# Kernel tuning notes

Measured on AMD Instinct MI355X. Metric: run time of the kernel, lower is better.

The kernel has to match this reference:

```python
import jax, jax.numpy as jnp
import numpy as np


def setup_inputs() -> dict:
    key = jax.random.key(0)
    k0, k1 = jax.random.split(key)
    B, C, H, W = 8, 16, 512, 512
    im0 = jax.random.normal(k0, (B, C, H, W), dtype=jnp.float32)
    flow = jax.random.normal(k1, (B, H, W, 2), dtype=jnp.float32)
    im1 = jnp.zeros((B, C, H, W), dtype=jnp.float32)
    return {"im0": im0, "flow": flow, "im1": im1}


def _forward_warp_bilinear(im0, flow, im1):
    # im0: [B,C,H,W], flow: [B,H,W,2] (flow[...,0]=dx, flow[...,1]=dy), im1: [B,C,H,W]
    B, C, H, W = im0.shape
    gx = jnp.arange(W, dtype=flow.dtype)[None, None, :]   # [1,1,W]
    gy = jnp.arange(H, dtype=flow.dtype)[None, :, None]   # [1,H,1]
    x = gx + flow[..., 0]                                 # [B,H,W] dest x
    y = gy + flow[..., 1]                                 # [B,H,W] dest y

    x0f = jnp.floor(x)
    y0f = jnp.floor(y)
    x0 = x0f.astype(jnp.int32)
    y0 = y0f.astype(jnp.int32)
    x1 = x0 + 1
    y1 = y0 + 1

    # Original Python/CUDA kernel scatters only if ALL four corners are in-bounds.
    valid = (x0 >= 0) & (x1 <= W - 1) & (y0 >= 0) & (y1 <= H - 1)  # [B,H,W]

    fx = x - x0f   # in [0,1)
    fy = y - y0f
    w_nw = (1.0 - fx) * (1.0 - fy)
    w_ne = fx * (1.0 - fy)
    w_sw = (1.0 - fx) * fy
    w_se = fx * fy

    # channel-last flat layout for efficient scatter: [B, H*W, C]
    src = jnp.transpose(im0, (0, 2, 3, 1)).reshape(B, H * W, C)
    out = jnp.transpose(im1, (0, 2, 3, 1)).reshape(B, H * W, C)
    bb = jnp.arange(B)[:, None]                            # [B,1] broadcasts over H*W

    for yi, xi, wgt in ((y0, x0, w_nw), (y0, x1, w_ne),
                        (y1, x0, w_sw), (y1, x1, w_se)):
        t = jnp.where(valid, yi * W + xi, 0).reshape(B, H * W)          # safe indices
        wv = jnp.where(valid, wgt, 0.0).reshape(B, H * W)               # zeroed weights
        out = out.at[bb, t].add(wv[..., None] * src)
    return jnp.transpose(out.reshape(B, H, W, C), (0, 3, 1, 2))


def reference(im0, flow, im1):
    return _forward_warp_bilinear(im0, flow, im1)
```

## Files before the change

### kernel.cpp

```cpp
#include <hip/hip_runtime.h>


#define BB 8
#define CC 16
#define HH 512
#define WW 512
#define TIL 32
#define RAD 4
#define REG (TIL + 2*RAD)
#define NSRC (REG*REG)
#define NTHR 512
#define NREC ((NSRC + NTHR - 1) / NTHR)
#define NENT (NSRC * 4)
#define CB 2
#define NGRP (CC / CB)

__global__ __launch_bounds__(NTHR, 6) void fwarp_tile(
    const float* __restrict__ im0,
    const float* __restrict__ flow,
    float* __restrict__ out)
{
    __shared__ unsigned s_ent[NENT];
    __shared__ unsigned s_cur[TIL * TIL];
    __shared__ float2   s_img[NSRC];
    __shared__ unsigned s_wtot[8];

    const int tid = threadIdx.x;
    const int bid  = blockIdx.x;
    const int tile = ((bid & 7) << 8) | (bid >> 3);
    const int tcx = tile & 15;
    const int tcy = (tile >> 4) & 15;
    const int b   = tile >> 8;
    const int w0  = tcx * TIL;
    const int h0  = tcy * TIL;

    const float2* flow2 = (const float2*)flow + ((size_t)b << 18);

    float4 rw[NREC];
    int    rp0[NREC];
    int    rk[NREC];
    int    rgi[NREC];

    for (int j = tid; j < TIL * TIL; j += NTHR) s_cur[j] = 0u;

#pragma unroll
    for (int r = 0; r < NREC; ++r) {
        rk[r] = 0; rp0[r] = 0; rgi[r] = 0;
        rw[r] = make_float4(0.f, 0.f, 0.f, 0.f);
        const int i = tid + r * NTHR;
        if (i < NSRC) {
            const int ry = i / REG;
            const int rx = i - ry * REG;
            const int sy = h0 - RAD + ry;
            const int sx = w0 - RAD + rx;
            const bool inimg = (sx >= 0) & (sx < WW) & (sy >= 0) & (sy < HH);
            rgi[r] = inimg ? ((sy << 9) + sx) : 0;

            float fxv = 0.0f, fyv = 0.0f;
            if (inimg) {
                const float2 f = flow2[(sy << 9) + sx];
                fxv = f.x; fyv = f.y;
            }
            const float x = (float)sx + fxv;
            const float y = (float)sy + fyv;
            const float x0f = floorf(x);
            const float y0f = floorf(y);
            const int x0 = (int)x0f;
            const int y0 = (int)y0f;

            const bool inrange = (fxv >= -(float)RAD) & (fxv < (float)RAD) &
                                 (fyv >= -(float)RAD) & (fyv < (float)RAD);
            const bool valid = inimg && inrange &&
                               (x0 >= 0) && (x0 <= WW - 2) && (y0 >= 0) && (y0 <= HH - 2);

            const float fx = x - x0f;
            const float fy = y - y0f;
            const int lx = x0 - w0;
            const int ly = y0 - h0;

            const bool okW = (lx >= 0)  & (lx < TIL);
            const bool okE = (lx >= -1) & (lx < TIL - 1);
            const bool okN = (ly >= 0)  & (ly < TIL);
            const bool okS = (ly >= -1) & (ly < TIL - 1);

            const float wnw = (1.0f - fx) * (1.0f - fy);
            const float wne = fx * (1.0f - fy);
            const float wsw = (1.0f - fx) * fy;
            const float wse = fx * fy;

            int m = 0;
            if (valid && okN && okW && (wnw != 0.0f)) m |= 1;
            if (valid && okN && okE && (wne != 0.0f)) m |= 2;
            if (valid && okS && okW && (wsw != 0.0f)) m |= 4;
            if (valid && okS && okE && (wse != 0.0f)) m |= 8;

            rk[r]  = m;
            rp0[r] = ly * TIL + lx;
            rw[r]  = make_float4(wnw, wne, wsw, wse);
        }
    }
    __syncthreads();

#pragma unroll
    for (int r = 0; r < NREC; ++r) {
        const int m = rk[r];
        const int p0 = rp0[r];
        if (m & 1) atomicAdd(&s_cur[p0], 1u);
        if (m & 2) atomicAdd(&s_cur[p0 + 1], 1u);
        if (m & 4) atomicAdd(&s_cur[p0 + TIL], 1u);
        if (m & 8) atomicAdd(&s_cur[p0 + TIL + 1], 1u);
    }
    __syncthreads();

    {
        const int lane = tid & 63;
        const int wv   = tid >> 6;
        const unsigned ca = s_cur[tid * 2 + 0];
        const unsigned cb = s_cur[tid * 2 + 1];
        const unsigned mysum = ca + cb;
        unsigned inc = mysum;
#pragma unroll
        for (int d = 1; d < 64; d <<= 1) {
            const unsigned u = __shfl_up(inc, d);
            if (lane >= d) inc += u;
        }
        if (lane == 63) s_wtot[wv] = inc;
        __syncthreads();
        unsigned wpre = 0;
#pragma unroll
        for (int w = 0; w < 7; ++w) if (wv > w) wpre += s_wtot[w];
        const unsigned o0 = wpre + inc - mysum;
        const unsigned o1 = o0 + ca;
        s_cur[tid * 2 + 0] = o0;
        s_cur[tid * 2 + 1] = o1;
    }
    __syncthreads();

    int rbeg[2], rend[2];
#pragma unroll
    for (int k = 0; k < 2; ++k) rbeg[k] = (int)s_cur[tid + k * NTHR];
    __syncthreads();

#pragma unroll
    for (int r = 0; r < NREC; ++r) {
        const int i = tid + r * NTHR;
        const int m = rk[r];
        const int p0 = rp0[r];
        const float4 w4 = rw[r];
        if (m & 1) { const unsigned s = atomicAdd(&s_cur[p0],           1u);
                     s_ent[s] = ((unsigned)i << 16) | (unsigned)(w4.x * 65535.0f + 0.5f); }
        if (m & 2) { const unsigned s = atomicAdd(&s_cur[p0 + 1],       1u);
                     s_ent[s] = ((unsigned)i << 16) | (unsigned)(w4.y * 65535.0f + 0.5f); }
        if (m & 4) { const unsigned s = atomicAdd(&s_cur[p0 + TIL],     1u);
                     s_ent[s] = ((unsigned)i << 16) | (unsigned)(w4.z * 65535.0f + 0.5f); }
        if (m & 8) { const unsigned s = atomicAdd(&s_cur[p0 + TIL + 1], 1u);
                     s_ent[s] = ((unsigned)i << 16) | (unsigned)(w4.w * 65535.0f + 0.5f); }
    }
    __syncthreads();
#pragma unroll
    for (int k = 0; k < 2; ++k) rend[k] = (int)s_cur[tid + k * NTHR];

    const float* imb = im0 + ((size_t)(b * CC) << 18);
    float* outb      = out + ((size_t)(b * CC) << 18);

    float2 vimg[NREC];

    {
        const float* p0c = imb;
        const float* p1c = imb + ((size_t)1 << 18);
#pragma unroll
        for (int r = 0; r < NREC; ++r) {
            const int i = tid + r * NTHR;
            if (i < NSRC) { vimg[r].x = p0c[rgi[r]]; vimg[r].y = p1c[rgi[r]]; }
        }
    }

    for (int g = 0; g < NGRP; ++g) {
        __syncthreads();
#pragma unroll
        for (int r = 0; r < NREC; ++r) {
            const int i = tid + r * NTHR;
            if (i < NSRC) s_img[i] = vimg[r];
        }
        __syncthreads();

        if (g + 1 < NGRP) {
            const float* p0c = imb + ((size_t)((g + 1) * CB) << 18);
            const float* p1c = imb + ((size_t)((g + 1) * CB + 1) << 18);
#pragma unroll
            for (int r = 0; r < NREC; ++r) {
                const int i = tid + r * NTHR;
                if (i < NSRC) { vimg[r].x = p0c[rgi[r]]; vimg[r].y = p1c[rgi[r]]; }
            }
        }

#pragma unroll
        for (int k = 0; k < 2; ++k) {
            const int p   = tid + k * NTHR;
            const int beg = rbeg[k];
            const int end = rend[k];

            float a0 = 0.f, a1 = 0.f;
            for (int j = beg; j < end; ++j) {
                const unsigned e = s_ent[j];
                const int   sp = (int)(e >> 16);
                const float w  = (float)(e & 0xFFFFu) * (1.0f / 65535.0f);
                const float2 v = s_img[sp];
                a0 = fmaf(w, v.x, a0);
                a1 = fmaf(w, v.y, a1);
            }

            const int dy = p >> 5;
            const int dx = p & 31;
            float* op = outb + ((size_t)(g * CB) << 18) + ((h0 + dy) << 9) + (w0 + dx);
            op[0]               = a0;
            op[(size_t)1 << 18] = a1;
        }
    }
}

__global__ __launch_bounds__(256) void fwarp_fallback(
    const float* __restrict__ im0,
    const float* __restrict__ flow,
    float* __restrict__ out)
{
    const int t = blockIdx.x * blockDim.x + threadIdx.x;
    const int idx0 = t << 2;

    const float4 fA = ((const float4*)flow)[(t << 1)];
    const float4 fB = ((const float4*)flow)[(t << 1) + 1];
    const float pfx[4] = {fA.x, fA.z, fB.x, fB.z};
    const float pfy[4] = {fA.y, fA.w, fB.y, fB.w};

#pragma unroll
    for (int k = 0; k < 4; ++k) {
        const float fxv = pfx[k];
        const float fyv = pfy[k];
        const bool inrange = (fxv >= -(float)RAD) & (fxv < (float)RAD) &
                             (fyv >= -(float)RAD) & (fyv < (float)RAD);
        if (inrange) continue;

        const int idx = idx0 + k;
        const int w = idx & (WW - 1);
        const int h = (idx >> 9) & (HH - 1);
        const int b = idx >> 18;

        const float x = (float)w + fxv;
        const float y = (float)h + fyv;
        const float x0f = floorf(x);
        const float y0f = floorf(y);
        const int x0 = (int)x0f;
        const int y0 = (int)y0f;
        if (x0 < 0 || x0 > WW - 2 || y0 < 0 || y0 > HH - 2) continue;

        const float fx = x - x0f;
        const float fy = y - y0f;
        const float wnw = (1.0f - fx) * (1.0f - fy);
        const float wne = fx * (1.0f - fy);
        const float wsw = (1.0f - fx) * fy;
        const float wse = fx * fy;

        const size_t plane = (size_t)HH * WW;
        const float* srcb = im0 + (size_t)b * CC * plane + (size_t)h * WW + w;
        float* dstb       = out + (size_t)b * CC * plane;
        const int o = y0 * WW + x0;

#pragma unroll
        for (int c = 0; c < CC; ++c) {
            const float v = srcb[c * plane];
            float* dc = dstb + c * plane;
            atomicAdd(dc + o,          v * wnw);
            atomicAdd(dc + o + 1,      v * wne);
            atomicAdd(dc + o + WW,     v * wsw);
            atomicAdd(dc + o + WW + 1, v * wse);
        }
    }
}

extern "C" void kernel_launch(void* const* d_in, const int* in_sizes, int n_in,
                              void* d_out, int out_size, void* d_ws, size_t ws_size,
                              hipStream_t stream) {
    const float* im0  = (const float*)d_in[0];
    const float* flow = (const float*)d_in[1];
    float* out = (float*)d_out;

    const int n_tiles = BB * (HH / TIL) * (WW / TIL);
    fwarp_tile<<<n_tiles, NTHR, 0, stream>>>(im0, flow, out);

    const int n_pix = BB * HH * WW;
    fwarp_fallback<<<n_pix / (256 * 4), 256, 0, stream>>>(im0, flow, out);
}
```

Before: 327.0 us.

## Gather four channels per pass with packed 16-bit counters and interleaved loops

```diff
diff --git a/kernel.cpp b/kernel.cpp
--- a/kernel.cpp
+++ b/kernel.cpp
@@ -12,8 +12,9 @@
 #define NTHR 512
 #define NREC ((NSRC + NTHR - 1) / NTHR)
 #define NENT (NSRC * 4)
-#define CB 2
+#define CB 4
 #define NGRP (CC / CB)
+#define NPIX (TIL * TIL)
 
 __global__ __launch_bounds__(NTHR, 6) void fwarp_tile(
     const float* __restrict__ im0,
@@ -21,8 +22,8 @@
     float* __restrict__ out)
 {
     __shared__ unsigned s_ent[NENT];
-    __shared__ unsigned s_cur[TIL * TIL];
-    __shared__ float2   s_img[NSRC];
+    __shared__ unsigned s_cur[NPIX / 2];
+    __shared__ float4   s_img[NSRC];
     __shared__ unsigned s_wtot[8];
 
     const int tid = threadIdx.x;
@@ -41,7 +42,7 @@
     int    rk[NREC];
     int    rgi[NREC];
 
-    for (int j = tid; j < TIL * TIL; j += NTHR) s_cur[j] = 0u;
+    for (int j = tid; j < NPIX / 2; j += NTHR) s_cur[j] = 0u;
 
 #pragma unroll
     for (int r = 0; r < NREC; ++r) {
@@ -105,19 +106,20 @@
     for (int r = 0; r < NREC; ++r) {
         const int m = rk[r];
         const int p0 = rp0[r];
-        if (m & 1) atomicAdd(&s_cur[p0], 1u);
-        if (m & 2) atomicAdd(&s_cur[p0 + 1], 1u);
-        if (m & 4) atomicAdd(&s_cur[p0 + TIL], 1u);
-        if (m & 8) atomicAdd(&s_cur[p0 + TIL + 1], 1u);
+        if (m & 1) { const int p = p0;           atomicAdd(&s_cur[p >> 1], 1u << ((p & 1) * 16)); }
+        if (m & 2) { const int p = p0 + 1;       atomicAdd(&s_cur[p >> 1], 1u << ((p & 1) * 16)); }
+        if (m & 4) { const int p = p0 + TIL;     atomicAdd(&s_cur[p >> 1], 1u << ((p & 1) * 16)); }
+        if (m & 8) { const int p = p0 + TIL + 1; atomicAdd(&s_cur[p >> 1], 1u << ((p & 1) * 16)); }
     }
     __syncthreads();
 
     {
         const int lane = tid & 63;
         const int wv   = tid >> 6;
-        const unsigned ca = s_cur[tid * 2 + 0];
-        const unsigned cb = s_cur[tid * 2 + 1];
-        const unsigned mysum = ca + cb;
+        const unsigned word = s_cur[tid];
+        const unsigned clo = word & 0xFFFFu;
+        const unsigned chi = word >> 16;
+        const unsigned mysum = clo + chi;
         unsigned inc = mysum;
 #pragma unroll
         for (int d = 1; d < 64; d <<= 1) {
@@ -129,16 +131,18 @@
         unsigned wpre = 0;
 #pragma unroll
         for (int w = 0; w < 7; ++w) if (wv > w) wpre += s_wtot[w];
-        const unsigned o0 = wpre + inc - mysum;
-        const unsigned o1 = o0 + ca;
-        s_cur[tid * 2 + 0] = o0;
-        s_cur[tid * 2 + 1] = o1;
+        const unsigned olo = wpre + inc - mysum;
+        const unsigned ohi = olo + clo;
+        s_cur[tid] = olo | (ohi << 16);
     }
     __syncthreads();
 
     int rbeg[2], rend[2];
 #pragma unroll
-    for (int k = 0; k < 2; ++k) rbeg[k] = (int)s_cur[tid + k * NTHR];
+    for (int k = 0; k < 2; ++k) {
+        const int p = tid + k * NTHR;
+        rbeg[k] = (int)((s_cur[p >> 1] >> ((p & 1) * 16)) & 0xFFFFu);
+    }
     __syncthreads();
 
 #pragma unroll
@@ -147,31 +151,46 @@
         const int m = rk[r];
         const int p0 = rp0[r];
         const float4 w4 = rw[r];
-        if (m & 1) { const unsigned s = atomicAdd(&s_cur[p0],           1u);
-                     s_ent[s] = ((unsigned)i << 16) | (unsigned)(w4.x * 65535.0f + 0.5f); }
-        if (m & 2) { const unsigned s = atomicAdd(&s_cur[p0 + 1],       1u);
-                     s_ent[s] = ((unsigned)i << 16) | (unsigned)(w4.y * 65535.0f + 0.5f); }
-        if (m & 4) { const unsigned s = atomicAdd(&s_cur[p0 + TIL],     1u);
-                     s_ent[s] = ((unsigned)i << 16) | (unsigned)(w4.z * 65535.0f + 0.5f); }
-        if (m & 8) { const unsigned s = atomicAdd(&s_cur[p0 + TIL + 1], 1u);
-                     s_ent[s] = ((unsigned)i << 16) | (unsigned)(w4.w * 65535.0f + 0.5f); }
-    }
-    __syncthreads();
-#pragma unroll
-    for (int k = 0; k < 2; ++k) rend[k] = (int)s_cur[tid + k * NTHR];
+        if (m & 1) { const int p = p0;
+            const unsigned old = atomicAdd(&s_cur[p >> 1], 1u << ((p & 1) * 16));
+            const unsigned s = (old >> ((p & 1) * 16)) & 0xFFFFu;
+            s_ent[s] = ((unsigned)i << 16) | (unsigned)(w4.x * 65535.0f + 0.5f); }
+        if (m & 2) { const int p = p0 + 1;
+            const unsigned old = atomicAdd(&s_cur[p >> 1], 1u << ((p & 1) * 16));
+            const unsigned s = (old >> ((p & 1) * 16)) & 0xFFFFu;
+            s_ent[s] = ((unsigned)i << 16) | (unsigned)(w4.y * 65535.0f + 0.5f); }
+        if (m & 4) { const int p = p0 + TIL;
+            const unsigned old = atomicAdd(&s_cur[p >> 1], 1u << ((p & 1) * 16));
+            const unsigned s = (old >> ((p & 1) * 16)) & 0xFFFFu;
+            s_ent[s] = ((unsigned)i << 16) | (unsigned)(w4.z * 65535.0f + 0.5f); }
+        if (m & 8) { const int p = p0 + TIL + 1;
+            const unsigned old = atomicAdd(&s_cur[p >> 1], 1u << ((p & 1) * 16));
+            const unsigned s = (old >> ((p & 1) * 16)) & 0xFFFFu;
+            s_ent[s] = ((unsigned)i << 16) | (unsigned)(w4.w * 65535.0f + 0.5f); }
+    }
+    __syncthreads();
+#pragma unroll
+    for (int k = 0; k < 2; ++k) {
+        const int p = tid + k * NTHR;
+        rend[k] = (int)((s_cur[p >> 1] >> ((p & 1) * 16)) & 0xFFFFu);
+    }
 
     const float* imb = im0 + ((size_t)(b * CC) << 18);
     float* outb      = out + ((size_t)(b * CC) << 18);
 
-    float2 vimg[NREC];
+    float4 vimg[NREC];
 
     {
-        const float* p0c = imb;
-        const float* p1c = imb + ((size_t)1 << 18);
+        const float* c0 = imb;
 #pragma unroll
         for (int r = 0; r < NREC; ++r) {
             const int i = tid + r * NTHR;
-            if (i < NSRC) { vimg[r].x = p0c[rgi[r]]; vimg[r].y = p1c[rgi[r]]; }
+            if (i < NSRC) {
+                vimg[r].x = c0[rgi[r]];
+                vimg[r].y = c0[((size_t)1 << 18) + rgi[r]];
+                vimg[r].z = c0[((size_t)2 << 18) + rgi[r]];
+                vimg[r].w = c0[((size_t)3 << 18) + rgi[r]];
+            }
         }
     }
 
@@ -185,36 +204,63 @@
         __syncthreads();
 
         if (g + 1 < NGRP) {
-            const float* p0c = imb + ((size_t)((g + 1) * CB) << 18);
-            const float* p1c = imb + ((size_t)((g + 1) * CB + 1) << 18);
+            const float* c0 = imb + ((size_t)((g + 1) * CB) << 18);
 #pragma unroll
             for (int r = 0; r < NREC; ++r) {
                 const int i = tid + r * NTHR;
-                if (i < NSRC) { vimg[r].x = p0c[rgi[r]]; vimg[r].y = p1c[rgi[r]]; }
-            }
-        }
-
-#pragma unroll
-        for (int k = 0; k < 2; ++k) {
-            const int p   = tid + k * NTHR;
-            const int beg = rbeg[k];
-            const int end = rend[k];
-
-            float a0 = 0.f, a1 = 0.f;
-            for (int j = beg; j < end; ++j) {
-                const unsigned e = s_ent[j];
-                const int   sp = (int)(e >> 16);
+                if (i < NSRC) {
+                    vimg[r].x = c0[rgi[r]];
+                    vimg[r].y = c0[((size_t)1 << 18) + rgi[r]];
+                    vimg[r].z = c0[((size_t)2 << 18) + rgi[r]];
+                    vimg[r].w = c0[((size_t)3 << 18) + rgi[r]];
+                }
+            }
+        }
+
+        int j0 = rbeg[0], j1 = rbeg[1];
+        const int e0 = rend[0], e1 = rend[1];
+        float4 a0 = make_float4(0.f, 0.f, 0.f, 0.f);
+        float4 a1 = make_float4(0.f, 0.f, 0.f, 0.f);
+        while ((j0 < e0) | (j1 < e1)) {
+            if (j0 < e0) {
+                const unsigned e = s_ent[j0++];
                 const float w  = (float)(e & 0xFFFFu) * (1.0f / 65535.0f);
-                const float2 v = s_img[sp];
-                a0 = fmaf(w, v.x, a0);
-                a1 = fmaf(w, v.y, a1);
-            }
-
+                const float4 v = s_img[e >> 16];
+                a0.x = fmaf(w, v.x, a0.x);
+                a0.y = fmaf(w, v.y, a0.y);
+                a0.z = fmaf(w, v.z, a0.z);
+                a0.w = fmaf(w, v.w, a0.w);
+            }
+            if (j1 < e1) {
+                const unsigned e = s_ent[j1++];
+                const float w  = (float)(e & 0xFFFFu) * (1.0f / 65535.0f);
+                const float4 v = s_img[e >> 16];
+                a1.x = fmaf(w, v.x, a1.x);
+                a1.y = fmaf(w, v.y, a1.y);
+                a1.z = fmaf(w, v.z, a1.z);
+                a1.w = fmaf(w, v.w, a1.w);
+            }
+        }
+
+        {
+            const int p  = tid;
             const int dy = p >> 5;
             const int dx = p & 31;
             float* op = outb + ((size_t)(g * CB) << 18) + ((h0 + dy) << 9) + (w0 + dx);
-            op[0]               = a0;
-            op[(size_t)1 << 18] = a1;
+            op[0]               = a0.x;
+            op[(size_t)1 << 18] = a0.y;
+            op[(size_t)2 << 18] = a0.z;
+            op[(size_t)3 << 18] = a0.w;
+        }
+        {
+            const int p  = tid + NTHR;
+            const int dy = p >> 5;
+            const int dx = p & 31;
+            float* op = outb + ((size_t)(g * CB) << 18) + ((h0 + dy) << 9) + (w0 + dx);
+            op[0]               = a1.x;
+            op[(size_t)1 << 18] = a1.y;
+            op[(size_t)2 << 18] = a1.z;
+            op[(size_t)3 << 18] = a1.w;
         }
     }
 }
```

Measured after the change: 326.4 us. About the same (-0.2%).
